# Kernel optimization log

Hardware: AMD Instinct MI355X
Metric: run time of the kernel (lower is better)

Reference implementation:

```python
import jax, jax.numpy as jnp
import numpy as np

NUM_USER = 1_000_000
EMBED_DIM = 64
N_GROUPS = 262144
GROUP_SIZE = 3  # fixed: prediction Linear(3,1) implies C(3,2)=3 pairs


def setup_inputs() -> dict:
    key = jax.random.key(0)
    k_g, k_e, k_w1, k_b1, k_w2, k_b2, k_wp, k_bp = jax.random.split(key, 8)
    group = jax.random.randint(k_g, (N_GROUPS, GROUP_SIZE), 0, NUM_USER)
    embed_table = jax.random.normal(k_e, (NUM_USER, EMBED_DIM), dtype=jnp.float32) * 0.02
    W1 = jax.random.normal(k_w1, (EMBED_DIM, 4), dtype=jnp.float32) * 0.1
    b1 = jax.random.normal(k_b1, (4,), dtype=jnp.float32) * 0.1
    W2 = jax.random.normal(k_w2, (4, 1), dtype=jnp.float32) * 0.1
    b2 = jax.random.normal(k_b2, (1,), dtype=jnp.float32) * 0.1
    Wp = jax.random.normal(k_wp, (3, 1), dtype=jnp.float32) * 0.1
    bp = jax.random.normal(k_bp, (1,), dtype=jnp.float32) * 0.1
    return {"group": group, "embed_table": embed_table, "W1": W1, "b1": b1,
            "W2": W2, "b2": b2, "Wp": Wp, "bp": bp}


def reference(group, embed_table, W1, b1, W2, b2, Wp, bp):
    # gather: [G, 3, D]
    gr = embed_table[group]
    # pairwise products in loop order (0,1),(0,2),(1,2): [G, 3, D]
    i_idx = jnp.array([0, 0, 1])
    j_idx = jnp.array([1, 2, 2])
    v_ij = gr[:, i_idx, :] * gr[:, j_idx, :]
    # attention MLP: Linear(D,4) -> sigmoid -> Linear(4,1) -> [G, 3]
    h = jax.nn.sigmoid(jnp.einsum('gpd,df->gpf', v_ij, W1) + b1)
    a = (jnp.einsum('gpf,fo->gpo', h, W2) + b2)[..., 0]  # [G, 3]
    # prediction Linear(3,1), then sigmoid*2-1 -> [G, 1]
    out = a @ Wp + bp
    return jax.nn.sigmoid(out) * 2.0 - 1.0
```

## Files before the change

kernel.cpp:

```cpp
#include <hip/hip_runtime.h>
#include <math.h>


static constexpr int G_TOTAL = 262144;

__device__ __forceinline__ float sigf(float x) {
    return 1.0f / (1.0f + expf(-x));
}

__device__ __forceinline__ float4 mlp_partial(const float4 v,
                                              const float4 w0, const float4 w1,
                                              const float4 w2, const float4 w3) {
    float4 r;
    r.x = fmaf(v.x, w0.x, fmaf(v.y, w1.x, fmaf(v.z, w2.x, v.w * w3.x)));
    r.y = fmaf(v.x, w0.y, fmaf(v.y, w1.y, fmaf(v.z, w2.y, v.w * w3.y)));
    r.z = fmaf(v.x, w0.z, fmaf(v.y, w1.z, fmaf(v.z, w2.z, v.w * w3.z)));
    r.w = fmaf(v.x, w0.w, fmaf(v.y, w1.w, fmaf(v.z, w2.w, v.w * w3.w)));
    return r;
}

__global__ __launch_bounds__(256) void afm_kernel(
    const int*   __restrict__ group,
    const float* __restrict__ embed,
    const float* __restrict__ W1,
    const float* __restrict__ b1,
    const float* __restrict__ W2,
    const float* __restrict__ b2,
    const float* __restrict__ Wp,
    const float* __restrict__ bp,
    float*       __restrict__ out)
{
    const int tid  = blockIdx.x * 256 + threadIdx.x;
    const int lane = threadIdx.x & 63;
    const int sub  = lane >> 4;
    const int l    = lane & 15;
    const int g    = (tid >> 6) * 4 + sub;

    const int base = g * 3;
    const int i0 = group[base + 0];
    const int i1 = group[base + 1];
    const int i2 = group[base + 2];

    const float4 e0 = ((const float4*)(embed + (size_t)i0 * 64))[l];
    const float4 e1 = ((const float4*)(embed + (size_t)i1 * 64))[l];
    const float4 e2 = ((const float4*)(embed + (size_t)i2 * 64))[l];

    const float4* w1v = (const float4*)W1 + (l << 2);
    const float4 wr0 = w1v[0];
    const float4 wr1 = w1v[1];
    const float4 wr2 = w1v[2];
    const float4 wr3 = w1v[3];

    float4 v;
    v.x = e0.x * e1.x; v.y = e0.y * e1.y; v.z = e0.z * e1.z; v.w = e0.w * e1.w;
    float4 acc01 = mlp_partial(v, wr0, wr1, wr2, wr3);
    v.x = e0.x * e2.x; v.y = e0.y * e2.y; v.z = e0.z * e2.z; v.w = e0.w * e2.w;
    float4 acc02 = mlp_partial(v, wr0, wr1, wr2, wr3);
    v.x = e1.x * e2.x; v.y = e1.y * e2.y; v.z = e1.z * e2.z; v.w = e1.w * e2.w;
    float4 acc12 = mlp_partial(v, wr0, wr1, wr2, wr3);

#pragma unroll
    for (int m = 8; m >= 1; m >>= 1) {
        acc01.x += __shfl_xor(acc01.x, m);
        acc01.y += __shfl_xor(acc01.y, m);
        acc01.z += __shfl_xor(acc01.z, m);
        acc01.w += __shfl_xor(acc01.w, m);
        acc02.x += __shfl_xor(acc02.x, m);
        acc02.y += __shfl_xor(acc02.y, m);
        acc02.z += __shfl_xor(acc02.z, m);
        acc02.w += __shfl_xor(acc02.w, m);
        acc12.x += __shfl_xor(acc12.x, m);
        acc12.y += __shfl_xor(acc12.y, m);
        acc12.z += __shfl_xor(acc12.z, m);
        acc12.w += __shfl_xor(acc12.w, m);
    }

    const float b10 = b1[0], b11 = b1[1], b12 = b1[2], b13 = b1[3];
    const float w20 = W2[0], w21 = W2[1], w22 = W2[2], w23 = W2[3];
    const float b2v = b2[0];

    float a0 = b2v + sigf(acc01.x + b10) * w20 + sigf(acc01.y + b11) * w21
                   + sigf(acc01.z + b12) * w22 + sigf(acc01.w + b13) * w23;
    float a1 = b2v + sigf(acc02.x + b10) * w20 + sigf(acc02.y + b11) * w21
                   + sigf(acc02.z + b12) * w22 + sigf(acc02.w + b13) * w23;
    float a2 = b2v + sigf(acc12.x + b10) * w20 + sigf(acc12.y + b11) * w21
                   + sigf(acc12.z + b12) * w22 + sigf(acc12.w + b13) * w23;

    const float z = bp[0] + a0 * Wp[0] + a1 * Wp[1] + a2 * Wp[2];
    const float res = 2.0f / (1.0f + expf(-z)) - 1.0f;

    if (l == 0) out[g] = res;
}

extern "C" void kernel_launch(void* const* d_in, const int* in_sizes, int n_in,
                              void* d_out, int out_size, void* d_ws, size_t ws_size,
                              hipStream_t stream) {
    const int*   group = (const int*)  d_in[0];
    const float* embed = (const float*)d_in[1];
    const float* W1    = (const float*)d_in[2];
    const float* b1    = (const float*)d_in[3];
    const float* W2    = (const float*)d_in[4];
    const float* b2    = (const float*)d_in[5];
    const float* Wp    = (const float*)d_in[6];
    const float* bp    = (const float*)d_in[7];
    float* out = (float*)d_out;

    afm_kernel<<<G_TOTAL / 16, 256, 0, stream>>>(
        group, embed, W1, b1, W2, b2, Wp, bp, out);
}
```

Baseline: 337.0 us.

## Assign four threads per group with shared-memory indices and W1

Each group is now handled by 4 threads instead of 16, so a block covers 64 groups. Each thread loads four float4 chunks per embedding row, interleaved so consecutive threads read adjacent 16-byte pieces. Group indices and W1 are staged in shared memory once per block, which cuts redundant global index loads and the shuffle reduction from 4 steps to 2. The trade-off is more registers and serial FMAs per thread, plus a block-level sync.

```diff
diff --git a/kernel.cpp b/kernel.cpp
--- a/kernel.cpp
+++ b/kernel.cpp
@@ -3,20 +3,10 @@
 
 
 static constexpr int G_TOTAL = 262144;
+static constexpr int GPB = 64;
 
 __device__ __forceinline__ float sigf(float x) {
     return 1.0f / (1.0f + expf(-x));
-}
-
-__device__ __forceinline__ float4 mlp_partial(const float4 v,
-                                              const float4 w0, const float4 w1,
-                                              const float4 w2, const float4 w3) {
-    float4 r;
-    r.x = fmaf(v.x, w0.x, fmaf(v.y, w1.x, fmaf(v.z, w2.x, v.w * w3.x)));
-    r.y = fmaf(v.x, w0.y, fmaf(v.y, w1.y, fmaf(v.z, w2.y, v.w * w3.y)));
-    r.z = fmaf(v.x, w0.z, fmaf(v.y, w1.z, fmaf(v.z, w2.z, v.w * w3.z)));
-    r.w = fmaf(v.x, w0.w, fmaf(v.y, w1.w, fmaf(v.z, w2.w, v.w * w3.w)));
-    return r;
 }
 
 __global__ __launch_bounds__(256) void afm_kernel(
@@ -30,37 +20,62 @@
     const float* __restrict__ bp,
     float*       __restrict__ out)
 {
-    const int tid  = blockIdx.x * 256 + threadIdx.x;
-    const int lane = threadIdx.x & 63;
-    const int sub  = lane >> 4;
-    const int l    = lane & 15;
-    const int g    = (tid >> 6) * 4 + sub;
+    __shared__ int    s_idx[GPB * 3];
+    __shared__ float4 s_w1[64];
 
-    const int base = g * 3;
-    const int i0 = group[base + 0];
-    const int i1 = group[base + 1];
-    const int i2 = group[base + 2];
+    const int t = threadIdx.x;
 
-    const float4 e0 = ((const float4*)(embed + (size_t)i0 * 64))[l];
-    const float4 e1 = ((const float4*)(embed + (size_t)i1 * 64))[l];
-    const float4 e2 = ((const float4*)(embed + (size_t)i2 * 64))[l];
+    if (t < GPB * 3) s_idx[t] = group[blockIdx.x * (GPB * 3) + t];
+    if (t < 64)      s_w1[t] = ((const float4*)W1)[t];
+    __syncthreads();
 
-    const float4* w1v = (const float4*)W1 + (l << 2);
-    const float4 wr0 = w1v[0];
-    const float4 wr1 = w1v[1];
-    const float4 wr2 = w1v[2];
-    const float4 wr3 = w1v[3];
+    const int sub = t >> 2;
+    const int l   = t & 3;
+    const int g   = blockIdx.x * GPB + sub;
 
-    float4 v;
-    v.x = e0.x * e1.x; v.y = e0.y * e1.y; v.z = e0.z * e1.z; v.w = e0.w * e1.w;
-    float4 acc01 = mlp_partial(v, wr0, wr1, wr2, wr3);
-    v.x = e0.x * e2.x; v.y = e0.y * e2.y; v.z = e0.z * e2.z; v.w = e0.w * e2.w;
-    float4 acc02 = mlp_partial(v, wr0, wr1, wr2, wr3);
-    v.x = e1.x * e2.x; v.y = e1.y * e2.y; v.z = e1.z * e2.z; v.w = e1.w * e2.w;
-    float4 acc12 = mlp_partial(v, wr0, wr1, wr2, wr3);
+    const int i0 = s_idx[sub * 3 + 0];
+    const int i1 = s_idx[sub * 3 + 1];
+    const int i2 = s_idx[sub * 3 + 2];
+
+    const float4* p0 = (const float4*)(embed + (size_t)i0 * 64);
+    const float4* p1 = (const float4*)(embed + (size_t)i1 * 64);
+    const float4* p2 = (const float4*)(embed + (size_t)i2 * 64);
+
+    float4 e0[4], e1[4], e2[4];
+#pragma unroll
+    for (int j = 0; j < 4; ++j) {
+        e0[j] = p0[j * 4 + l];
+        e1[j] = p1[j * 4 + l];
+        e2[j] = p2[j * 4 + l];
+    }
+
+    float4 acc01 = {0,0,0,0}, acc02 = {0,0,0,0}, acc12 = {0,0,0,0};
+#pragma unroll
+    for (int j = 0; j < 4; ++j) {
+        const float4 a = e0[j], b = e1[j], c = e2[j];
+        const float v01[4] = {a.x*b.x, a.y*b.y, a.z*b.z, a.w*b.w};
+        const float v02[4] = {a.x*c.x, a.y*c.y, a.z*c.z, a.w*c.w};
+        const float v12[4] = {b.x*c.x, b.y*c.y, b.z*c.z, b.w*c.w};
+#pragma unroll
+        for (int k = 0; k < 4; ++k) {
+            const float4 w = s_w1[j * 16 + l * 4 + k];
+            acc01.x = fmaf(v01[k], w.x, acc01.x);
+            acc01.y = fmaf(v01[k], w.y, acc01.y);
+            acc01.z = fmaf(v01[k], w.z, acc01.z);
+            acc01.w = fmaf(v01[k], w.w, acc01.w);
+            acc02.x = fmaf(v02[k], w.x, acc02.x);
+            acc02.y = fmaf(v02[k], w.y, acc02.y);
+            acc02.z = fmaf(v02[k], w.z, acc02.z);
+            acc02.w = fmaf(v02[k], w.w, acc02.w);
+            acc12.x = fmaf(v12[k], w.x, acc12.x);
+            acc12.y = fmaf(v12[k], w.y, acc12.y);
+            acc12.z = fmaf(v12[k], w.z, acc12.z);
+            acc12.w = fmaf(v12[k], w.w, acc12.w);
+        }
+    }
 
 #pragma unroll
-    for (int m = 8; m >= 1; m >>= 1) {
+    for (int m = 2; m >= 1; m >>= 1) {
         acc01.x += __shfl_xor(acc01.x, m);
         acc01.y += __shfl_xor(acc01.y, m);
         acc01.z += __shfl_xor(acc01.z, m);
@@ -75,16 +90,16 @@
         acc12.w += __shfl_xor(acc12.w, m);
     }
 
-    const float b10 = b1[0], b11 = b1[1], b12 = b1[2], b13 = b1[3];
+    const float b10 = b1[0], b11 = b1[1], b12v = b1[2], b13 = b1[3];
     const float w20 = W2[0], w21 = W2[1], w22 = W2[2], w23 = W2[3];
     const float b2v = b2[0];
 
-    float a0 = b2v + sigf(acc01.x + b10) * w20 + sigf(acc01.y + b11) * w21
-                   + sigf(acc01.z + b12) * w22 + sigf(acc01.w + b13) * w23;
-    float a1 = b2v + sigf(acc02.x + b10) * w20 + sigf(acc02.y + b11) * w21
-                   + sigf(acc02.z + b12) * w22 + sigf(acc02.w + b13) * w23;
-    float a2 = b2v + sigf(acc12.x + b10) * w20 + sigf(acc12.y + b11) * w21
-                   + sigf(acc12.z + b12) * w22 + sigf(acc12.w + b13) * w23;
+    const float a0 = b2v + sigf(acc01.x + b10) * w20 + sigf(acc01.y + b11) * w21
+                         + sigf(acc01.z + b12v) * w22 + sigf(acc01.w + b13) * w23;
+    const float a1 = b2v + sigf(acc02.x + b10) * w20 + sigf(acc02.y + b11) * w21
+                         + sigf(acc02.z + b12v) * w22 + sigf(acc02.w + b13) * w23;
+    const float a2 = b2v + sigf(acc12.x + b10) * w20 + sigf(acc12.y + b11) * w21
+                         + sigf(acc12.z + b12v) * w22 + sigf(acc12.w + b13) * w23;
 
     const float z = bp[0] + a0 * Wp[0] + a1 * Wp[1] + a2 * Wp[2];
     const float res = 2.0f / (1.0f + expf(-z)) - 1.0f;
@@ -105,6 +120,6 @@
     const float* bp    = (const float*)d_in[7];
     float* out = (float*)d_out;
 
-    afm_kernel<<<G_TOTAL / 16, 256, 0, stream>>>(
+    afm_kernel<<<G_TOTAL / GPB, 256, 0, stream>>>(
         group, embed, W1, b1, W2, b2, Wp, bp, out);
 }
```

Result: no change. 336.2 us, median of 2 (-0.2%).
